# Kernel optimization log

Hardware: AMD Instinct MI355X
Metric: run time of the kernel (lower is better)

## Reference

```python
import jax, jax.numpy as jnp
import numpy as np

EPS = 1e-12  # matches F.normalize default eps

def _l2norm(x):
    n = jnp.linalg.norm(x, axis=-1, keepdims=True)
    return x / jnp.maximum(n, EPS)

def setup_inputs() -> dict:
    key = jax.random.key(0)
    kq, kk, kv = jax.random.split(key, 3)
    B, N, D = 16384, 8192, 1024
    return {
        "query": jax.random.normal(kq, (B, D), dtype=jnp.float32),
        "keys": jax.random.normal(kk, (N, D), dtype=jnp.float32),
        "values": jax.random.normal(kv, (N, D), dtype=jnp.float32),
        "k": 4,
    }

def reference(query, keys, values, k):
    # cosine similarity: (B, N)
    qn = _l2norm(query)
    kn = _l2norm(keys)
    sim = jnp.einsum('bd,nd->bn', qn, kn)
    actual_k = min(k, sim.shape[1])
    topk_sim, topk_idx = jax.lax.top_k(sim, actual_k)     # (B, k)
    weights = jax.nn.softmax(topk_sim, axis=-1)            # (B, k)
    topk_vals = values[topk_idx]                           # (B, k, D)
    return jnp.einsum('bk,bkd->bd', weights, topk_vals)    # (B, D)
```

## Files before the change

### kernel.cpp

```cpp
#include <hip/hip_runtime.h>
#include <hip/hip_bf16.h>
#include <math.h>


#define D_DIM 1024
#define SLICES 4
#define BQ 128
#define BK 128
#define BD 64
#define TLIST 4
#define CAND_PER_Q (SLICES * 2 * 4 * TLIST)

typedef float f32x4 __attribute__((ext_vector_type(4)));
typedef short s16x8 __attribute__((ext_vector_type(8)));

typedef const __attribute__((address_space(1))) void* as1cv;
typedef __attribute__((address_space(3))) void* as3v;

__device__ __forceinline__ void gload_lds16(const void* g, void* l) {
    __builtin_amdgcn_global_load_lds((as1cv)g, (as3v)l, 16, 0, 0);
}

__device__ __forceinline__ unsigned short f2bf(float x) {
    unsigned int u;
    __builtin_memcpy(&u, &x, 4);
    unsigned int r = (u + 0x7fffu + ((u >> 16) & 1u)) >> 16;
    return (unsigned short)r;
}

__global__ __launch_bounds__(256) void nrm_kernel(
    const float* __restrict__ q, const float* __restrict__ kmat,
    unsigned short* __restrict__ qn, unsigned short* __restrict__ kn,
    float* __restrict__ inv_qn, float* __restrict__ inv_kn, int B, int N) {
    int wid = threadIdx.x >> 6, lane = threadIdx.x & 63;
    int row = blockIdx.x * 4 + wid;
    if (row >= B + N) return;
    const float* src;
    unsigned short* dst;
    float* invp;
    if (row < B) {
        src = q + (size_t)row * D_DIM; dst = qn + (size_t)row * D_DIM; invp = inv_qn + row;
    } else {
        int r = row - B;
        src = kmat + (size_t)r * D_DIM; dst = kn + (size_t)r * D_DIM; invp = inv_kn + r;
    }
    float4 v[4];
    float ss = 0.f;
#pragma unroll
    for (int c = 0; c < 4; ++c) {
        v[c] = *(const float4*)(src + c * 256 + lane * 4);
        ss += v[c].x * v[c].x + v[c].y * v[c].y + v[c].z * v[c].z + v[c].w * v[c].w;
    }
#pragma unroll
    for (int m = 1; m < 64; m <<= 1) ss += __shfl_xor(ss, m, 64);
    float s = 1.0f / fmaxf(sqrtf(ss), 1e-12f);
    if (lane == 0) *invp = s;
#pragma unroll
    for (int c = 0; c < 4; ++c) {
        ushort4 o;
        o.x = f2bf(v[c].x * s); o.y = f2bf(v[c].y * s);
        o.z = f2bf(v[c].z * s); o.w = f2bf(v[c].w * s);
        *(ushort4*)(dst + c * 256 + lane * 4) = o;
    }
}

__global__ __launch_bounds__(256, 2) void score_kernel(
    const unsigned short* __restrict__ qn, const unsigned short* __restrict__ kn,
    float* __restrict__ cand_s, int* __restrict__ cand_i, int B, int N) {
    __shared__ __attribute__((aligned(16))) unsigned short Kt[BK * BD];
    __shared__ __attribute__((aligned(16))) unsigned short Qt[BQ * BD];
    int bx = blockIdx.x;
    int qblk = bx >> 2, slice = bx & 3;
    int tid = threadIdx.x, wid = tid >> 6, lane = tid & 63;
    int wr = wid & 1, wc = wid >> 1;
    int slice_len = N / SLICES;
    int kbase0 = slice * slice_len;
    int qbase = qblk * BQ;

    float ts[4][TLIST];
    int   ti[4][TLIST];
#pragma unroll
    for (int cg = 0; cg < 4; ++cg)
#pragma unroll
        for (int t = 0; t < TLIST; ++t) { ts[cg][t] = -1e30f; ti[cg][t] = 0; }

    for (int kt = 0; kt < slice_len / BK; ++kt) {
        int kb = kbase0 + kt * BK;
        f32x4 acc[4][4];
#pragma unroll
        for (int a = 0; a < 4; ++a)
#pragma unroll
            for (int b = 0; b < 4; ++b) acc[a][b] = (f32x4){0.f, 0.f, 0.f, 0.f};

        for (int dc = 0; dc < D_DIM / BD; ++dc) {
            int db = dc * BD;
#pragma unroll
            for (int i = 0; i < 4; ++i) {
                int te = (i * 4 + wid) * 64 + lane;
                int r = te >> 3, sl = te & 7;
                int c = (sl ^ (r & 7)) * 8;
                gload_lds16(kn + (size_t)(kb + r) * D_DIM + db + c, &Kt[(i * 4 + wid) * 512]);
            }
#pragma unroll
            for (int i = 0; i < 4; ++i) {
                int te = (i * 4 + wid) * 64 + lane;
                int r = te >> 3, sl = te & 7;
                int c = (sl ^ (r & 7)) * 8;
                gload_lds16(qn + (size_t)(qbase + r) * D_DIM + db + c, &Qt[(i * 4 + wid) * 512]);
            }
            __syncthreads();
#pragma unroll
            for (int ks = 0; ks < 2; ++ks) {
                int kslot = ks * 4 + (lane >> 4);
                s16x8 afr[4], bfr[4];
#pragma unroll
                for (int rb = 0; rb < 4; ++rb) {
                    int row = wr * 64 + rb * 16 + (lane & 15);
                    afr[rb] = *(const s16x8*)&Kt[row * BD + ((kslot ^ (row & 7)) * 8)];
                }
#pragma unroll
                for (int cg = 0; cg < 4; ++cg) {
                    int row = wc * 64 + cg * 16 + (lane & 15);
                    bfr[cg] = *(const s16x8*)&Qt[row * BD + ((kslot ^ (row & 7)) * 8)];
                }
#pragma unroll
                for (int rb = 0; rb < 4; ++rb)
#pragma unroll
                    for (int cg = 0; cg < 4; ++cg)
                        acc[rb][cg] = __builtin_amdgcn_mfma_f32_16x16x32_bf16(
                            afr[rb], bfr[cg], acc[rb][cg], 0, 0, 0);
            }
            __syncthreads();
        }
#pragma unroll
        for (int rb = 0; rb < 4; ++rb) {
#pragma unroll
            for (int j = 0; j < 4; ++j) {
                int key = kb + wr * 64 + rb * 16 + ((lane >> 4) << 2) + j;
#pragma unroll
                for (int cg = 0; cg < 4; ++cg) {
                    float s = acc[rb][cg][j];
                    if (s > ts[cg][TLIST - 1]) {
                        int id = key;
#pragma unroll
                        for (int t = 0; t < TLIST; ++t) {
                            bool c = s > ts[cg][t];
                            float hi = c ? s : ts[cg][t];
                            float lo = c ? ts[cg][t] : s;
                            int ih = c ? id : ti[cg][t];
                            int il = c ? ti[cg][t] : id;
                            ts[cg][t] = hi; ti[cg][t] = ih; s = lo; id = il;
                        }
                    }
                }
            }
        }
    }
#pragma unroll
    for (int cg = 0; cg < 4; ++cg) {
        int qg = qbase + wc * 64 + cg * 16 + (lane & 15);
        int lg = lane >> 4;
        size_t base = (size_t)qg * CAND_PER_Q + slice * (2 * 4 * TLIST) + wr * (4 * TLIST) + lg * TLIST;
#pragma unroll
        for (int t = 0; t < TLIST; ++t) {
            cand_s[base + t] = ts[cg][t];
            cand_i[base + t] = ti[cg][t];
        }
    }
}

__global__ __launch_bounds__(256) void final_kernel(
    const float* __restrict__ q, const float* __restrict__ kmat, const float* __restrict__ vmat,
    const float* __restrict__ inv_qn, const float* __restrict__ inv_kn,
    const float* __restrict__ cand_s, const int* __restrict__ cand_i,
    const int* __restrict__ kptr, float* __restrict__ out, int B, int N) {
    int qi = blockIdx.x;
    int tid = threadIdx.x, lane = tid & 63, wid = tid >> 6;
    __shared__ int sel[8];
    __shared__ float exsc[8];
    __shared__ float wgt[8];
    __shared__ int widx[8];
    int kk = *kptr;
    kk = kk < 1 ? 1 : (kk > 8 ? 8 : kk);

    if (wid == 0) {
        size_t cb = (size_t)qi * CAND_PER_Q;
        float s0 = cand_s[cb + lane], s1 = cand_s[cb + 64 + lane];
        int i0 = cand_i[cb + lane], i1 = cand_i[cb + 64 + lane];
        if (s1 > s0) { float tf = s0; s0 = s1; s1 = tf; int tt = i0; i0 = i1; i1 = tt; }
        for (int it = 0; it < 8; ++it) {
            float v = s0; int ki = i0; int ln = lane;
#pragma unroll
            for (int m = 1; m < 64; m <<= 1) {
                float ov = __shfl_xor(v, m, 64);
                int oki = __shfl_xor(ki, m, 64);
                int oln = __shfl_xor(ln, m, 64);
                if (ov > v || (ov == v && oki < ki)) { v = ov; ki = oki; ln = oln; }
            }
            if (lane == ln) { s0 = s1; i0 = i1; s1 = -1e30f; }
            if (lane == 0) sel[it] = ki;
        }
    }
    __syncthreads();

    int c = tid >> 5, l5 = tid & 31;
    const float* qrow = q + (size_t)qi * D_DIM;
    int kidx = sel[c];
    const float* krow = kmat + (size_t)kidx * D_DIM;
    float p = 0.f;
#pragma unroll
    for (int e = 0; e < 32; ++e) {
        int d = e * 32 + l5;
        p += qrow[d] * krow[d];
    }
#pragma unroll
    for (int m = 1; m < 32; m <<= 1) p += __shfl_xor(p, m, 64);
    if (l5 == 0) exsc[c] = p * inv_qn[qi] * inv_kn[kidx];
    __syncthreads();

    if (tid == 0) {
        float sc[8]; int id[8]; bool used[8];
#pragma unroll
        for (int i = 0; i < 8; ++i) { sc[i] = exsc[i]; id[i] = sel[i]; used[i] = false; }
        float wl[8]; int il[8];
        for (int i = 0; i < kk; ++i) {
            int bj = 0; float bv = -1e30f; int bi = 0x7fffffff;
            for (int j = 0; j < 8; ++j) {
                if (!used[j] && (sc[j] > bv || (sc[j] == bv && id[j] < bi))) {
                    bv = sc[j]; bi = id[j]; bj = j;
                }
            }
            used[bj] = true; wl[i] = bv; il[i] = bi;
        }
        float m0 = wl[0], ssum = 0.f;
        for (int i = 0; i < kk; ++i) { wl[i] = expf(wl[i] - m0); ssum += wl[i]; }
        for (int i = 0; i < kk; ++i) { wgt[i] = wl[i] / ssum; widx[i] = il[i]; }
    }
    __syncthreads();

    int d0 = tid * 4;
    float4 o = {0.f, 0.f, 0.f, 0.f};
    for (int i = 0; i < kk; ++i) {
        const float4 vv = *(const float4*)(vmat + (size_t)widx[i] * D_DIM + d0);
        float wi = wgt[i];
        o.x += wi * vv.x; o.y += wi * vv.y; o.z += wi * vv.z; o.w += wi * vv.w;
    }
    *(float4*)(out + (size_t)qi * D_DIM + d0) = o;
}

extern "C" void kernel_launch(void* const* d_in, const int* in_sizes, int n_in,
                              void* d_out, int out_size, void* d_ws, size_t ws_size,
                              hipStream_t stream) {
    const float* q = (const float*)d_in[0];
    const float* kmat = (const float*)d_in[1];
    const float* vmat = (const float*)d_in[2];
    const int* kptr = (const int*)d_in[3];
    float* out = (float*)d_out;
    int B = in_sizes[0] / D_DIM;
    int N = in_sizes[1] / D_DIM;

    char* ws = (char*)d_ws;
    size_t off = 0;
    unsigned short* qn = (unsigned short*)(ws + off); off += (size_t)B * D_DIM * 2;
    unsigned short* kn = (unsigned short*)(ws + off); off += (size_t)N * D_DIM * 2;
    float* inv_qn = (float*)(ws + off); off += (size_t)B * 4;
    float* inv_kn = (float*)(ws + off); off += (size_t)N * 4;
    float* cand_s = (float*)(ws + off); off += (size_t)B * CAND_PER_Q * 4;
    int* cand_i = (int*)(ws + off); off += (size_t)B * CAND_PER_Q * 4;

    int rows = B + N;
    nrm_kernel<<<dim3((rows + 3) / 4), dim3(256), 0, stream>>>(q, kmat, qn, kn, inv_qn, inv_kn, B, N);
    score_kernel<<<dim3((B / BQ) * SLICES), dim3(256), 0, stream>>>(qn, kn, cand_s, cand_i, B, N);
    final_kernel<<<dim3(B), dim3(256), 0, stream>>>(q, kmat, vmat, inv_qn, inv_kn,
                                                    cand_s, cand_i, kptr, out, B, N);
}
```

Before: 677.0 us.

## Merge candidates in-block, double key slices, and use one wave per query in final kernel

The score kernel now splits keys into 8 slices instead of 4 and asks for 4 blocks per SM in its launch bounds. Each block merges its 32 per-thread top-4 lists through shared memory into one top-4 per query before writing, which cuts candidate traffic to 32 per query. The final kernel maps one wave to each query, using register shuffles in place of shared-memory syncs and a single-thread serial section. The cost is an extra in-block merge with two barriers, and the tighter launch bounds may cause register pressure or spills in the MFMA loop.

New measurement: 687.0 us. No clear change (+1.5%).

```diff
diff --git a/kernel.cpp b/kernel.cpp
--- a/kernel.cpp
+++ b/kernel.cpp
@@ -4,12 +4,12 @@
 
 
 #define D_DIM 1024
-#define SLICES 4
+#define SLICES 8
 #define BQ 128
 #define BK 128
 #define BD 64
 #define TLIST 4
-#define CAND_PER_Q (SLICES * 2 * 4 * TLIST)
+#define CAND_PER_Q (SLICES * TLIST)
 
 typedef float f32x4 __attribute__((ext_vector_type(4)));
 typedef short s16x8 __attribute__((ext_vector_type(8)));
@@ -64,18 +64,23 @@
     }
 }
 
-__global__ __launch_bounds__(256, 2) void score_kernel(
+__global__ __launch_bounds__(256, 4) void score_kernel(
     const unsigned short* __restrict__ qn, const unsigned short* __restrict__ kn,
     float* __restrict__ cand_s, int* __restrict__ cand_i, int B, int N) {
-    __shared__ __attribute__((aligned(16))) unsigned short Kt[BK * BD];
-    __shared__ __attribute__((aligned(16))) unsigned short Qt[BQ * BD];
+    __shared__ __attribute__((aligned(16))) unsigned char smem[33792];
+    unsigned short* Kt = (unsigned short*)smem;
+    unsigned short* Qt = (unsigned short*)(smem + 16384);
+    float* ms = (float*)smem;
+    int* mi = (int*)(smem + 16896);
+
     int bx = blockIdx.x;
-    int qblk = bx >> 2, slice = bx & 3;
+    int qblk = bx >> 3, slice = bx & 7;
     int tid = threadIdx.x, wid = tid >> 6, lane = tid & 63;
     int wr = wid & 1, wc = wid >> 1;
     int slice_len = N / SLICES;
     int kbase0 = slice * slice_len;
     int qbase = qblk * BQ;
+    int lg = lane >> 4;
 
     float ts[4][TLIST];
     int   ti[4][TLIST];
@@ -111,7 +116,7 @@
             __syncthreads();
 #pragma unroll
             for (int ks = 0; ks < 2; ++ks) {
-                int kslot = ks * 4 + (lane >> 4);
+                int kslot = ks * 4 + lg;
                 s16x8 afr[4], bfr[4];
 #pragma unroll
                 for (int rb = 0; rb < 4; ++rb) {
@@ -136,7 +141,7 @@
         for (int rb = 0; rb < 4; ++rb) {
 #pragma unroll
             for (int j = 0; j < 4; ++j) {
-                int key = kb + wr * 64 + rb * 16 + ((lane >> 4) << 2) + j;
+                int key = kb + wr * 64 + rb * 16 + (lg << 2) + j;
 #pragma unroll
                 for (int cg = 0; cg < 4; ++cg) {
                     float s = acc[rb][cg][j];
@@ -156,15 +161,43 @@
             }
         }
     }
+
+    __syncthreads();
 #pragma unroll
     for (int cg = 0; cg < 4; ++cg) {
-        int qg = qbase + wc * 64 + cg * 16 + (lane & 15);
-        int lg = lane >> 4;
-        size_t base = (size_t)qg * CAND_PER_Q + slice * (2 * 4 * TLIST) + wr * (4 * TLIST) + lg * TLIST;
+        int ql = wc * 64 + cg * 16 + (lane & 15);
+        int slot = wr * 16 + lg * 4;
 #pragma unroll
         for (int t = 0; t < TLIST; ++t) {
-            cand_s[base + t] = ts[cg][t];
-            cand_i[base + t] = ti[cg][t];
+            ms[ql * 33 + slot + t] = ts[cg][t];
+            mi[ql * 33 + slot + t] = ti[cg][t];
+        }
+    }
+    __syncthreads();
+    if (tid < BQ) {
+        float bs[4] = {-1e30f, -1e30f, -1e30f, -1e30f};
+        int bi4[4] = {0, 0, 0, 0};
+#pragma unroll
+        for (int s = 0; s < 32; ++s) {
+            float v = ms[tid * 33 + s];
+            int id = mi[tid * 33 + s];
+            if (v > bs[3]) {
+#pragma unroll
+                for (int t = 0; t < 4; ++t) {
+                    bool c = v > bs[t];
+                    float hi = c ? v : bs[t];
+                    float lo = c ? bs[t] : v;
+                    int ih = c ? id : bi4[t];
+                    int il = c ? bi4[t] : id;
+                    bs[t] = hi; bi4[t] = ih; v = lo; id = il;
+                }
+            }
+        }
+        size_t base = (size_t)(qbase + tid) * CAND_PER_Q + slice * TLIST;
+#pragma unroll
+        for (int t = 0; t < 4; ++t) {
+            cand_s[base + t] = bs[t];
+            cand_i[base + t] = bi4[t];
         }
     }
 }
@@ -174,78 +207,90 @@
     const float* __restrict__ inv_qn, const float* __restrict__ inv_kn,
     const float* __restrict__ cand_s, const int* __restrict__ cand_i,
     const int* __restrict__ kptr, float* __restrict__ out, int B, int N) {
-    int qi = blockIdx.x;
-    int tid = threadIdx.x, lane = tid & 63, wid = tid >> 6;
-    __shared__ int sel[8];
-    __shared__ float exsc[8];
-    __shared__ float wgt[8];
-    __shared__ int widx[8];
+    int wid = threadIdx.x >> 6, lane = threadIdx.x & 63;
+    int qi = blockIdx.x * 4 + wid;
     int kk = *kptr;
     kk = kk < 1 ? 1 : (kk > 8 ? 8 : kk);
 
-    if (wid == 0) {
-        size_t cb = (size_t)qi * CAND_PER_Q;
-        float s0 = cand_s[cb + lane], s1 = cand_s[cb + 64 + lane];
-        int i0 = cand_i[cb + lane], i1 = cand_i[cb + 64 + lane];
-        if (s1 > s0) { float tf = s0; s0 = s1; s1 = tf; int tt = i0; i0 = i1; i1 = tt; }
-        for (int it = 0; it < 8; ++it) {
-            float v = s0; int ki = i0; int ln = lane;
-#pragma unroll
-            for (int m = 1; m < 64; m <<= 1) {
-                float ov = __shfl_xor(v, m, 64);
-                int oki = __shfl_xor(ki, m, 64);
-                int oln = __shfl_xor(ln, m, 64);
-                if (ov > v || (ov == v && oki < ki)) { v = ov; ki = oki; ln = oln; }
-            }
-            if (lane == ln) { s0 = s1; i0 = i1; s1 = -1e30f; }
-            if (lane == 0) sel[it] = ki;
-        }
-    }
-    __syncthreads();
-
-    int c = tid >> 5, l5 = tid & 31;
+    size_t cb = (size_t)qi * CAND_PER_Q;
+    float live = lane < 32 ? cand_s[cb + lane] : -1e30f;
+    int ci = lane < 32 ? cand_i[cb + lane] : 0;
+
+    int sel[8];
+#pragma unroll
+    for (int it = 0; it < 8; ++it) {
+        float v = live; int ln = lane;
+#pragma unroll
+        for (int m = 1; m < 64; m <<= 1) {
+            float ov = __shfl_xor(v, m, 64);
+            int oln = __shfl_xor(ln, m, 64);
+            if (ov > v || (ov == v && oln < ln)) { v = ov; ln = oln; }
+        }
+        sel[it] = __shfl(ci, ln, 64);
+        if (lane == ln) live = -1e30f;
+    }
+
     const float* qrow = q + (size_t)qi * D_DIM;
-    int kidx = sel[c];
-    const float* krow = kmat + (size_t)kidx * D_DIM;
-    float p = 0.f;
-#pragma unroll
-    for (int e = 0; e < 32; ++e) {
-        int d = e * 32 + l5;
-        p += qrow[d] * krow[d];
-    }
-#pragma unroll
-    for (int m = 1; m < 32; m <<= 1) p += __shfl_xor(p, m, 64);
-    if (l5 == 0) exsc[c] = p * inv_qn[qi] * inv_kn[kidx];
-    __syncthreads();
-
-    if (tid == 0) {
-        float sc[8]; int id[8]; bool used[8];
-#pragma unroll
-        for (int i = 0; i < 8; ++i) { sc[i] = exsc[i]; id[i] = sel[i]; used[i] = false; }
-        float wl[8]; int il[8];
-        for (int i = 0; i < kk; ++i) {
-            int bj = 0; float bv = -1e30f; int bi = 0x7fffffff;
-            for (int j = 0; j < 8; ++j) {
-                if (!used[j] && (sc[j] > bv || (sc[j] == bv && id[j] < bi))) {
-                    bv = sc[j]; bi = id[j]; bj = j;
-                }
-            }
-            used[bj] = true; wl[i] = bv; il[i] = bi;
-        }
-        float m0 = wl[0], ssum = 0.f;
-        for (int i = 0; i < kk; ++i) { wl[i] = expf(wl[i] - m0); ssum += wl[i]; }
-        for (int i = 0; i < kk; ++i) { wgt[i] = wl[i] / ssum; widx[i] = il[i]; }
-    }
-    __syncthreads();
-
-    int d0 = tid * 4;
-    float4 o = {0.f, 0.f, 0.f, 0.f};
-    for (int i = 0; i < kk; ++i) {
-        const float4 vv = *(const float4*)(vmat + (size_t)widx[i] * D_DIM + d0);
-        float wi = wgt[i];
-        o.x += wi * vv.x; o.y += wi * vv.y; o.z += wi * vv.z; o.w += wi * vv.w;
-    }
-    *(float4*)(out + (size_t)qi * D_DIM + d0) = o;
+    float4 qv[4];
+#pragma unroll
+    for (int c = 0; c < 4; ++c) qv[c] = *(const float4*)(qrow + c * 256 + lane * 4);
+    float invq = inv_qn[qi];
+    float exsc[8];
+#pragma unroll
+    for (int c = 0; c < 8; ++c) {
+        const float* krow = kmat + (size_t)sel[c] * D_DIM;
+        float p = 0.f;
+#pragma unroll
+        for (int e = 0; e < 4; ++e) {
+            float4 kv = *(const float4*)(krow + e * 256 + lane * 4);
+            p += qv[e].x * kv.x + qv[e].y * kv.y + qv[e].z * kv.z + qv[e].w * kv.w;
+        }
+#pragma unroll
+        for (int m = 1; m < 64; m <<= 1) p += __shfl_xor(p, m, 64);
+        exsc[c] = p * invq * inv_kn[sel[c]];
+    }
+
+    float wl[8]; int il[8]; bool used[8];
+#pragma unroll
+    for (int i = 0; i < 8; ++i) used[i] = false;
+#pragma unroll
+    for (int i = 0; i < 8; ++i) {
+        int bj = 0; float bv = -1e30f; int bidx = 0x7fffffff;
+#pragma unroll
+        for (int j = 0; j < 8; ++j) {
+            if (!used[j] && (exsc[j] > bv || (exsc[j] == bv && sel[j] < bidx))) {
+                bv = exsc[j]; bidx = sel[j]; bj = j;
+            }
+        }
+        used[bj] = true; wl[i] = bv; il[i] = bidx;
+    }
+    float m0 = wl[0], ssum = 0.f;
+#pragma unroll
+    for (int i = 0; i < 8; ++i) {
+        wl[i] = (i < kk) ? __expf(wl[i] - m0) : 0.f;
+        ssum += wl[i];
+    }
+    float rs = 1.0f / ssum;
+
+    float4 o[4];
+#pragma unroll
+    for (int c = 0; c < 4; ++c) o[c] = (float4){0.f, 0.f, 0.f, 0.f};
+#pragma unroll
+    for (int i = 0; i < 8; ++i) {
+        if (i < kk) {
+            const float* vrow = vmat + (size_t)il[i] * D_DIM;
+            float wi = wl[i] * rs;
+#pragma unroll
+            for (int c = 0; c < 4; ++c) {
+                float4 vv = *(const float4*)(vrow + c * 256 + lane * 4);
+                o[c].x += wi * vv.x; o[c].y += wi * vv.y;
+                o[c].z += wi * vv.z; o[c].w += wi * vv.w;
+            }
+        }
+    }
+    float* orow = out + (size_t)qi * D_DIM;
+#pragma unroll
+    for (int c = 0; c < 4; ++c) *(float4*)(orow + c * 256 + lane * 4) = o[c];
 }
 
 extern "C" void kernel_launch(void* const* d_in, const int* in_sizes, int n_in,
@@ -271,6 +316,6 @@
     int rows = B + N;
     nrm_kernel<<<dim3((rows + 3) / 4), dim3(256), 0, stream>>>(q, kmat, qn, kn, inv_qn, inv_kn, B, N);
     score_kernel<<<dim3((B / BQ) * SLICES), dim3(256), 0, stream>>>(qn, kn, cand_s, cand_i, B, N);
-    final_kernel<<<dim3(B), dim3(256), 0, stream>>>(q, kmat, vmat, inv_qn, inv_kn,
-                                                    cand_s, cand_i, kptr, out, B, N);
-}
+    final_kernel<<<dim3(B / 4), dim3(256), 0, stream>>>(q, kmat, vmat, inv_qn, inv_kn,
+                                                        cand_s, cand_i, kptr, out, B, N);
+}
```
